# Performance work log

Measured on AMD Instinct MI355X. Metric: run time of the kernel, lower is better.

The kernel has to match this reference:

```python
import jax, jax.numpy as jnp
import numpy as np
from jax import lax

EPS = 1e-5
B, CIN, H, W = 4, 512, 64, 64
CI = CIN // 4          # inter_channels = 128
CQK = CI // 8          # PAM query/key channels = 16
NC = 19                # num_classes


def conv2d(x, w, pad):
    return lax.conv_general_dilated(x, w, (1, 1), [(pad, pad), (pad, pad)],
                                    dimension_numbers=('NCHW', 'OIHW', 'NCHW'))


def bn_relu(x, g, b, m, v):
    # eval-mode BatchNorm2d followed by ReLU
    inv = g * lax.rsqrt(v + EPS)
    return jax.nn.relu(x * inv[None, :, None, None] + (b - m * inv)[None, :, None, None])


def setup_inputs() -> dict:
    key = jax.random.key(0)
    ks = iter(jax.random.split(key, 40))
    rn = lambda shape, s=0.02: (jax.random.normal(next(ks), shape, dtype=jnp.float32) * s)
    ones = lambda n: jnp.ones((n,), jnp.float32)
    zeros = lambda n: jnp.zeros((n,), jnp.float32)
    inp = {
        'x': jax.random.normal(next(ks), (B, CIN, H, W), dtype=jnp.float32),
        # conv_p1: 3x3 conv (no bias) + BN
        'wp1': rn((CI, CIN, 3, 3)),
        'bnp1_w': ones(CI), 'bnp1_b': zeros(CI), 'bnp1_m': zeros(CI), 'bnp1_v': ones(CI),
        # PAM 1x1 convs
        'qw': rn((CQK, CI, 1, 1)), 'qb': zeros(CQK),
        'kw': rn((CQK, CI, 1, 1)), 'kb': zeros(CQK),
        'vw': rn((CI, CI, 1, 1)), 'vb': zeros(CI),
        'pam_gamma': jnp.full((1,), 0.5, jnp.float32),
        # conv_p2
        'wp2': rn((CI, CI, 3, 3)),
        'bnp2_w': ones(CI), 'bnp2_b': zeros(CI), 'bnp2_m': zeros(CI), 'bnp2_v': ones(CI),
        # conv_c1
        'wc1': rn((CI, CIN, 3, 3)),
        'bnc1_w': ones(CI), 'bnc1_b': zeros(CI), 'bnc1_m': zeros(CI), 'bnc1_v': ones(CI),
        'cam_gamma': jnp.full((1,), 0.5, jnp.float32),
        # conv_c2
        'wc2': rn((CI, CI, 3, 3)),
        'bnc2_w': ones(CI), 'bnc2_b': zeros(CI), 'bnc2_m': zeros(CI), 'bnc2_v': ones(CI),
        # classifier heads (dropout is eval-mode identity)
        'cls_w': rn((NC, CI, 1, 1)), 'cls_b': zeros(NC),
        'auxp_w': rn((NC, CI, 1, 1)), 'auxp_b': zeros(NC),
        'auxc_w': rn((NC, CI, 1, 1)), 'auxc_b': zeros(NC),
    }
    return inp


def pam(x, qw, qb, kw, kb, vw, vb, gamma):
    b, c, h, w = x.shape
    n = h * w
    q = (conv2d(x, qw, 0) + qb[None, :, None, None]).reshape(b, -1, n)  # [B,CQK,N]
    k = (conv2d(x, kw, 0) + kb[None, :, None, None]).reshape(b, -1, n)  # [B,CQK,N]
    v = (conv2d(x, vw, 0) + vb[None, :, None, None]).reshape(b, c, n)   # [B,C,N]
    attn = jax.nn.softmax(jnp.einsum('bcn,bcm->bnm', q, k), axis=-1)    # [B,N,N]
    out = jnp.einsum('bcm,bnm->bcn', v, attn).reshape(b, c, h, w)
    return gamma * out + x


def cam(x, gamma):
    b, c, h, w = x.shape
    f = x.reshape(b, c, -1)                                             # [B,C,N]
    attn = jax.nn.softmax(jnp.einsum('bin,bjn->bij', f, f), axis=-1)    # [B,C,C]
    out = jnp.einsum('bij,bjn->bin', attn, f).reshape(b, c, h, w)
    return gamma * out + x


def _forward(x, wp1, bnp1_w, bnp1_b, bnp1_m, bnp1_v,
             qw, qb, kw, kb, vw, vb, pam_gamma,
             wp2, bnp2_w, bnp2_b, bnp2_m, bnp2_v,
             wc1, bnc1_w, bnc1_b, bnc1_m, bnc1_v, cam_gamma,
             wc2, bnc2_w, bnc2_b, bnc2_m, bnc2_v,
             cls_w, cls_b, auxp_w, auxp_b, auxc_w, auxc_b):
    feat_p = bn_relu(conv2d(x, wp1, 1), bnp1_w, bnp1_b, bnp1_m, bnp1_v)
    feat_p = pam(feat_p, qw, qb, kw, kb, vw, vb, pam_gamma)
    feat_p = bn_relu(conv2d(feat_p, wp2, 1), bnp2_w, bnp2_b, bnp2_m, bnp2_v)

    feat_c = bn_relu(conv2d(x, wc1, 1), bnc1_w, bnc1_b, bnc1_m, bnc1_v)
    feat_c = cam(feat_c, cam_gamma)
    feat_c = bn_relu(conv2d(feat_c, wc2, 1), bnc2_w, bnc2_b, bnc2_m, bnc2_v)

    feat = feat_p + feat_c
    out = conv2d(feat, cls_w, 0) + cls_b[None, :, None, None]
    out_p = conv2d(feat_p, auxp_w, 0) + auxp_b[None, :, None, None]
    out_c = conv2d(feat_c, auxc_w, 0) + auxc_b[None, :, None, None]
    return out, out_p, out_c


def reference(x, wp1, bnp1_w, bnp1_b, bnp1_m, bnp1_v,
              qw, qb, kw, kb, vw, vb, pam_gamma,
              wp2, bnp2_w, bnp2_b, bnp2_m, bnp2_v,
              wc1, bnc1_w, bnc1_b, bnc1_m, bnc1_v, cam_gamma,
              wc2, bnc2_w, bnc2_b, bnc2_m, bnc2_v,
              cls_w, cls_b, auxp_w, auxp_b, auxc_w, auxc_b):
    return _forward(x, wp1, bnp1_w, bnp1_b, bnp1_m, bnp1_v,
                    qw, qb, kw, kb, vw, vb, pam_gamma,
                    wp2, bnp2_w, bnp2_b, bnp2_m, bnp2_v,
                    wc1, bnc1_w, bnc1_b, bnc1_m, bnc1_v, cam_gamma,
                    wc2, bnc2_w, bnc2_b, bnc2_m, bnc2_v,
                    cls_w, cls_b, auxp_w, auxp_b, auxc_w, auxc_b)
```

## Files before the change

### kernel.cpp

```cpp
#include <hip/hip_runtime.h>
#include <cstdint>
#include <cstddef>


using s16x8 = __attribute__((ext_vector_type(8))) short;
using u16x8 = __attribute__((ext_vector_type(8))) unsigned short;
using u16x4 = __attribute__((ext_vector_type(4))) unsigned short;
using f32x4 = __attribute__((ext_vector_type(4))) float;
using f32x16 = __attribute__((ext_vector_type(16))) float;
using u32x4v = __attribute__((ext_vector_type(4))) unsigned;

__device__ __forceinline__ f32x4 mfma16(u16x8 a, u16x8 b, f32x4 c) {
  return __builtin_amdgcn_mfma_f32_16x16x32_bf16(
      __builtin_bit_cast(s16x8, a), __builtin_bit_cast(s16x8, b), c, 0, 0, 0);
}
__device__ __forceinline__ f32x16 mfma32(u16x8 a, u16x8 b, f32x16 c) {
  return __builtin_amdgcn_mfma_f32_32x32x16_bf16(
      __builtin_bit_cast(s16x8, a), __builtin_bit_cast(s16x8, b), c, 0, 0, 0);
}
__device__ __forceinline__ float bf2f(unsigned short u) {
  return __builtin_bit_cast(float, (unsigned)u << 16);
}
__device__ __forceinline__ unsigned short f2bf(float f) {
  unsigned u = __builtin_bit_cast(unsigned, f);
  u += 0x7fffu + ((u >> 16) & 1u);
  return (unsigned short)(u >> 16);
}
__device__ __forceinline__ unsigned cvt_pk_bf16(float lo, float hi) {
  unsigned r;
  asm("v_cvt_pk_bf16_f32 %0, %1, %2" : "=v"(r) : "v"(lo), "v"(hi));
  return r;
}
__device__ __forceinline__ u16x8 ld8(const unsigned short* p) {
  return *reinterpret_cast<const u16x8*>(p);
}
__device__ __forceinline__ void gload16(const void* g, void* l) {
  __builtin_amdgcn_global_load_lds(
      (const __attribute__((address_space(1))) void*)g,
      (__attribute__((address_space(3))) void*)l, 16, 0, 0);
}

#define OFF_XT    ((size_t)0)
#define OFF_FP1   ((size_t)19464192)
#define OFF_FC1   ((size_t)24330240)
#define OFF_FP0   ((size_t)29196288)
#define OFF_FC0   ((size_t)33390592)
#define OFF_FP2   ((size_t)37584896)
#define OFF_FC2   ((size_t)41779200)
#define OFF_WT1   ((size_t)45973504)
#define OFF_WT2   ((size_t)48332800)
#define OFF_QKW   ((size_t)48922624)
#define OFF_VWW   ((size_t)48930816)
#define OFF_HWW   ((size_t)48963584)
#define OFF_BNSS  ((size_t)48988160)
#define OFF_ATTN  ((size_t)48992256)
#define OFF_Q     OFF_FP2
#define OFF_K     (OFF_FP2 + 524288)
#define OFF_V     OFF_FC2

__device__ __forceinline__ int swzkey8(int col) {
  return ((col ^ (col >> 3)) & 7) << 3;
}

__global__ __launch_bounds__(256) void k_padzero(char* ws0) {
  const int img = blockIdx.x;
  unsigned short* base;
  if (img < 32)
    base = (unsigned short*)(ws0 + OFF_XT) + (size_t)img * 304128;
  else if (img < 40)
    base = (unsigned short*)(ws0 + OFF_FP1) + (size_t)(img - 32) * 304128;
  else
    base = (unsigned short*)(ws0 + OFF_FC1) + (size_t)(img - 40) * 304128;
  const u16x8 z = {0, 0, 0, 0, 0, 0, 0, 0};
#pragma unroll 1
  for (int it = 0; it < 21; ++it) {
    int idx = it * 256 + threadIdx.x;
    if (idx >= 5248) break;
    int cell = idx >> 3, part = idx & 7;
    int row, col;
    if (cell < 72) {
      row = 0; col = cell;
    } else if (cell < 144) {
      row = 65; col = cell - 72;
    } else {
      int q = cell - 144;
      row = 1 + (q >> 3);
      int cc = q & 7;
      col = cc ? (64 + cc) : 0;
    }
    *(u16x8*)(base + (size_t)(row * 72 + col) * 64 + part * 8) = z;
  }
}

__global__ __launch_bounds__(256) void k_xpose(const float* __restrict__ x,
                                               unsigned short* __restrict__ xt) {
  __shared__ float tile[128][65];
  const int t = threadIdx.x;
  const int blk = blockIdx.x;
  const int cb = blk & 3;
  const int h = (blk >> 2) & 63;
  const int b = blk >> 8;
  const float* src = x + ((size_t)(b * 512 + cb * 128) * 64 + h) * 64;
  const int w = t & 63, cr = t >> 6;
  for (int i = 0; i < 32; ++i) tile[cr + i * 4][w] = src[(size_t)(cr + i * 4) * 4096 + w];
  __syncthreads();
  const int w2 = t >> 2, cg = t & 3;
  const int cic = cb * 2 + (cg >> 1);
  const int col = w2 + 1;
  const int key8 = swzkey8(col);
  unsigned short* dst =
      xt + (((size_t)(b * 8 + cic) * 66 + h + 1) * 72 + col) * 64 + (cg & 1) * 32;
#pragma unroll
  for (int j = 0; j < 32; j += 4) {
    const int q0 = (cg & 1) * 32 + j;
    const int srow = (cg >> 1) * 64 + (q0 ^ key8);
    u16x4 pk;
    pk[0] = f2bf(tile[srow + 0][w2]);
    pk[1] = f2bf(tile[srow + 1][w2]);
    pk[2] = f2bf(tile[srow + 2][w2]);
    pk[3] = f2bf(tile[srow + 3][w2]);
    *reinterpret_cast<u16x4*>(dst + j) = pk;
  }
}

struct PackArgs {
  const float *wp1, *wc1, *wp2, *wc2, *qw, *kw, *vw, *clsw, *apw, *acw;
  const float *g1p, *b1p, *m1p, *v1p, *g1c, *b1c, *m1c, *v1c;
  const float *g2p, *b2p, *m2p, *v2p, *g2c, *b2c, *m2c, *v2c;
  unsigned short *wt1, *wt2, *qkw, *vww, *hww;
  float* bnss;
};
__global__ __launch_bounds__(256) void k_pack(PackArgs A) {
  const int i = blockIdx.x * 256 + threadIdx.x;
  const int N1 = 2 * 8 * 9 * 8192;
  const int N2 = N1 + 2 * 2 * 9 * 8192;
  const int N3 = N2 + 2 * 16 * 128;
  const int N4 = N3 + 128 * 128;
  const int N5 = N4 + 3 * 32 * 128;
  const int N6 = N5 + 8 * 128;
  if (i < N1) {
    int e = i & 7, ln = (i >> 3) & 63, q = (i >> 9) & 15;
    int rest = i >> 13;
    int tap = rest % 9, cc = rest / 9;
    int cic = cc & 7, brr = cc >> 3;
    const float* s = brr ? A.wc1 : A.wp1;
    int co = (q >> 2) * 32 + (ln & 31);
    int ci = (q & 3) * 16 + (ln >> 5) * 8 + e;
    A.wt1[i] = f2bf(s[(size_t)(co * 512 + cic * 64 + ci) * 9 + tap]);
  } else if (i < N2) {
    int k = i - N1;
    int e = k & 7, ln = (k >> 3) & 63, q = (k >> 9) & 15;
    int rest = k >> 13;
    int tap = rest % 9, cc = rest / 9;
    int cic = cc & 1, brr = cc >> 1;
    const float* s = brr ? A.wc2 : A.wp2;
    int co = (q >> 2) * 32 + (ln & 31);
    int ci = (q & 3) * 16 + (ln >> 5) * 8 + e;
    A.wt2[k] = f2bf(s[(size_t)(co * 128 + cic * 64 + ci) * 9 + tap]);
  } else if (i < N3) {
    int k = i - N2;
    int ci = k & 127, q = k >> 7;
    const float* s = (q < 16) ? A.qw : A.kw;
    A.qkw[k] = f2bf(s[(q & 15) * 128 + ci]);
  } else if (i < N4) {
    int k = i - N3;
    A.vww[k] = f2bf(A.vw[k]);
  } else if (i < N5) {
    int k = i - N4;
    int ci = k & 127, co = (k >> 7) & 31, hd = k >> 12;
    const float* s = hd == 0 ? A.clsw : (hd == 1 ? A.apw : A.acw);
    A.hww[k] = (co < 19) ? f2bf(s[co * 128 + ci]) : (unsigned short)0;
  } else if (i < N6) {
    int k = i - N5;
    int j = k & 127, seg = k >> 7;
    const float *g, *bb, *mm, *vv;
    switch (seg >> 1) {
      case 0: g = A.g1p; bb = A.b1p; mm = A.m1p; vv = A.v1p; break;
      case 1: g = A.g1c; bb = A.b1c; mm = A.m1c; vv = A.v1c; break;
      case 2: g = A.g2p; bb = A.b2p; mm = A.m2p; vv = A.v2p; break;
      default: g = A.g2c; bb = A.b2c; mm = A.m2c; vv = A.v2c; break;
    }
    float sc = g[j] * rsqrtf(vv[j] + 1e-5f);
    A.bnss[k] = (seg & 1) ? (bb[j] - mm[j] * sc) : sc;
  }
}

__device__ __forceinline__ void conv_stageA(const unsigned short* inp, int imgChunk,
                                            int h0, int gtid, char* db) {
  const char* sr = (const char*)(inp + (((size_t)imgChunk * 66 + h0) * 72) * 64);
#pragma unroll
  for (int i = 0; i < 9; ++i)
    gload16(sr + i * 4096 + gtid * 16, db + i * 4096 + gtid * 16);
}

__device__ __forceinline__ void conv_loadW(const unsigned short* wgrp, int Tl, int wq,
                                           int lane, u16x8 (&s)[8]) {
  const unsigned short* wtap = wgrp + (size_t)Tl * 8192;
#pragma unroll
  for (int j = 0; j < 8; ++j)
    s[j] = ld8(wtap + (size_t)(wq + j) * 512 + lane * 8);
}

__device__ __forceinline__ void conv_tap(const char* ab, const unsigned short* wr,
                                         int wq, int lane, int l31, int hi16, int rowb,
                                         int ty, int tx, bool rld, u16x8 (&bvc)[8],
                                         f32x16& a00, f32x16& a01, f32x16& a10,
                                         f32x16& a11) {
  int abase0, akey0, abase1, akey1;
  {
    int col = l31 + tx;
    abase0 = ((rowb + ty) * 72 + col) << 7;
    akey0 = ((col ^ (col >> 3)) & 7) << 4;
    int col1 = 32 + l31 + tx;
    abase1 = ((rowb + ty) * 72 + col1) << 7;
    akey1 = ((col1 ^ (col1 >> 3)) & 7) << 4;
  }
#pragma unroll
  for (int s = 0; s < 4; ++s) {
    const int ko = s * 32 + hi16;
    u16x8 av0 = *(const u16x8*)(ab + abase0 + (ko ^ akey0));
    u16x8 av1 = *(const u16x8*)(ab + abase1 + (ko ^ akey1));
    a00 = mfma32(av0, bvc[s], a00);
    a01 = mfma32(av0, bvc[4 + s], a01);
    a10 = mfma32(av1, bvc[s], a10);
    a11 = mfma32(av1, bvc[4 + s], a11);
    if (rld) {
      bvc[s] = ld8(wr + (size_t)(wq + s) * 512 + lane * 8);
      bvc[4 + s] = ld8(wr + (size_t)(wq + 4 + s) * 512 + lane * 8);
    }
  }
}

__device__ __forceinline__ void acc_to_lds(f32x4* cbuf, int base, int lane,
                                           const f32x16& v) {
#pragma unroll
  for (int jj = 0; jj < 4; ++jj) {
    f32x4 x = {v[4 * jj + 0], v[4 * jj + 1], v[4 * jj + 2], v[4 * jj + 3]};
    cbuf[(base + jj) * 64 + lane] = x;
  }
}
__device__ __forceinline__ void acc_from_lds(const f32x4* cbuf, int base, int lane,
                                             f32x16& v) {
#pragma unroll
  for (int jj = 0; jj < 4; ++jj) {
    f32x4 x = cbuf[(base + jj) * 64 + lane];
#pragma unroll
    for (int r = 0; r < 4; ++r) v[4 * jj + r] += x[r];
  }
}
__device__ __forceinline__ void conv_store(unsigned short* outp, size_t bbase, int h0,
                                           int nbase, int co, float sc, float sh,
                                           int hi, const f32x16& v) {
#pragma unroll
  for (int r = 0; r < 16; ++r) {
    int n = nbase + (r & 3) + 8 * (r >> 2) + 4 * hi;
    float y = v[r] * sc + sh;
    y = y > 0.f ? y : 0.f;
    outp[bbase + ((size_t)(h0 + (n >> 6)) * 64 + (n & 63)) * 128 + co] = f2bf(y);
  }
}

template <int NCHUNK>
__global__ __launch_bounds__(512, 1) void k_conv3x3(
    const unsigned short* __restrict__ in0, const unsigned short* __restrict__ in1,
    const unsigned short* __restrict__ wt, const float* __restrict__ bnb,
    unsigned short* __restrict__ out0, unsigned short* __restrict__ out1) {
  __shared__ unsigned short Awin[2 * 4 * 72 * 64];
  const int bid = blockIdx.x;
  const int ht = bid & 31;
  const int b = (bid >> 5) & 3;
  const int br = bid >> 7;
  const unsigned short* inp = br ? in1 : in0;
  const unsigned short* wbr = wt + (size_t)br * NCHUNK * 9 * 8192;
  const float* scale = bnb + br * 256;
  const float* shiftp = scale + 128;
  unsigned short* outp = br ? out1 : out0;
  const int tid = threadIdx.x;
  const int lane = tid & 63, wv = tid >> 6;
  const int l31 = lane & 31, hi = lane >> 5;
  const int hi16 = hi * 16;
  const int group = wv >> 2, w = wv & 3;
  const int wn = (w & 1) * 64, cob = (w >> 1) * 64;
  const int rowb = w & 1;
  const int h0 = ht * 2;
  const int CPG = NCHUNK / 2;
  const int TPG = CPG * 9;
  const int c0 = group * CPG;
  const unsigned short* wgrp = wbr + (size_t)c0 * 9 * 8192;
  const int gtid = tid & 255;
  const int wq = (w >> 1) * 8;
  char* myA = (char*)Awin + group * 36864;
  const int imgBase = b * NCHUNK + c0;

  f32x16 a00 = (f32x16)0.f, a01 = (f32x16)0.f, a10 = (f32x16)0.f, a11 = (f32x16)0.f;
  u16x8 bv0[8], bv1[8];

  conv_stageA(inp, imgBase, h0, gtid, myA);
  conv_loadW(wgrp, 0, wq, lane, bv0);
  if (TPG > 1) conv_loadW(wgrp, 1, wq, lane, bv1);
  asm volatile("s_waitcnt vmcnt(0)" ::: "memory");
  __builtin_amdgcn_s_barrier();

#pragma unroll 1
  for (int c = 0; c < CPG; c += 2) {
#pragma unroll
    for (int t = 0; t < 9; ++t) {
      const int Tl = c * 9 + t;
      const bool rld = (Tl + 2 < TPG);
      const unsigned short* wr = wgrp + (size_t)(Tl + 2) * 8192;
      const int ty = t / 3, tx = t - ty * 3;
      if ((t & 1) == 0)
        conv_tap(myA, wr, wq, lane, l31, hi16, rowb, ty, tx, rld, bv0, a00, a01, a10, a11);
      else
        conv_tap(myA, wr, wq, lane, l31, hi16, rowb, ty, tx, rld, bv1, a00, a01, a10, a11);
    }
    if (c + 1 < CPG) {
      asm volatile("s_waitcnt lgkmcnt(0)" ::: "memory");
      __builtin_amdgcn_s_barrier();
      conv_stageA(inp, imgBase + c + 1, h0, gtid, myA);
      asm volatile("s_waitcnt vmcnt(0)" ::: "memory");
      __builtin_amdgcn_s_barrier();
#pragma unroll
      for (int t = 0; t < 9; ++t) {
        const int Tl = (c + 1) * 9 + t;
        const bool rld = (Tl + 2 < TPG);
        const unsigned short* wr = wgrp + (size_t)(Tl + 2) * 8192;
        const int ty = t / 3, tx = t - ty * 3;
        if ((t & 1) == 0)
          conv_tap(myA, wr, wq, lane, l31, hi16, rowb, ty, tx, rld, bv1, a00, a01, a10,
                   a11);
        else
          conv_tap(myA, wr, wq, lane, l31, hi16, rowb, ty, tx, rld, bv0, a00, a01, a10,
                   a11);
      }
      if (c + 2 < CPG) {
        asm volatile("s_waitcnt lgkmcnt(0)" ::: "memory");
        __builtin_amdgcn_s_barrier();
        conv_stageA(inp, imgBase + c + 2, h0, gtid, myA);
        asm volatile("s_waitcnt vmcnt(0)" ::: "memory");
        __builtin_amdgcn_s_barrier();
      }
    }
  }

  asm volatile("s_waitcnt lgkmcnt(0)" ::: "memory");
  __builtin_amdgcn_s_barrier();
  f32x4* cbuf = (f32x4*)Awin;
  if (group == 1) {
    acc_to_lds(cbuf, w * 16 + 0, lane, a00);
    acc_to_lds(cbuf, w * 16 + 4, lane, a01);
    acc_to_lds(cbuf, w * 16 + 8, lane, a10);
    acc_to_lds(cbuf, w * 16 + 12, lane, a11);
  }
  asm volatile("s_waitcnt lgkmcnt(0)" ::: "memory");
  __builtin_amdgcn_s_barrier();
  if (group == 0) {
    acc_from_lds(cbuf, w * 16 + 0, lane, a00);
    acc_from_lds(cbuf, w * 16 + 4, lane, a01);
    acc_from_lds(cbuf, w * 16 + 8, lane, a10);
    acc_from_lds(cbuf, w * 16 + 12, lane, a11);
    const size_t bbase = (size_t)b * 4096 * 128;
    {
      const int co = cob + l31;
      const float sc = scale[co], sh = shiftp[co];
      conv_store(outp, bbase, h0, wn + 0, co, sc, sh, hi, a00);
      conv_store(outp, bbase, h0, wn + 32, co, sc, sh, hi, a10);
    }
    {
      const int co = cob + 32 + l31;
      const float sc = scale[co], sh = shiftp[co];
      conv_store(outp, bbase, h0, wn + 0, co, sc, sh, hi, a01);
      conv_store(outp, bbase, h0, wn + 32, co, sc, sh, hi, a11);
    }
  }
}

__global__ __launch_bounds__(256) void k_qkv(
    const unsigned short* __restrict__ fp0, const unsigned short* __restrict__ qkw,
    const unsigned short* __restrict__ vww, const float* __restrict__ qb,
    const float* __restrict__ kb, const float* __restrict__ vb,
    unsigned short* __restrict__ Q, unsigned short* __restrict__ K,
    unsigned short* __restrict__ V2) {
  const int bid = blockIdx.x;
  const int nt = bid & 63, b = bid >> 6;
  const int lane = threadIdx.x & 63, wv = threadIdx.x >> 6;
  const int lg = lane >> 4, l15 = lane & 15;
  const int n = nt * 64 + wv * 16 + l15;
  const unsigned short* fbase = fp0 + ((size_t)b * 4096 + n) * 128 + lg * 8;
  f32x4 vacc[8];
#pragma unroll
  for (int mf = 0; mf < 8; ++mf) vacc[mf] = (f32x4){0.f, 0.f, 0.f, 0.f};
  f32x4 qacc = {0.f, 0.f, 0.f, 0.f}, kacc = {0.f, 0.f, 0.f, 0.f};
#pragma unroll
  for (int kc = 0; kc < 128; kc += 32) {
    u16x8 fb = ld8(fbase + kc);
    u16x8 qa = ld8(qkw + (size_t)l15 * 128 + lg * 8 + kc);
    u16x8 ka = ld8(qkw + 2048 + (size_t)l15 * 128 + lg * 8 + kc);
    qacc = mfma16(qa, fb, qacc);
    kacc = mfma16(ka, fb, kacc);
#pragma unroll
    for (int mf = 0; mf < 8; ++mf) {
      u16x8 va = ld8(vww + (size_t)(mf * 16 + l15) * 128 + lg * 8 + kc);
      vacc[mf] = mfma16(va, fb, vacc[mf]);
    }
  }
  const float LOG2E = 1.44269504088896f;
#pragma unroll
  for (int r = 0; r < 4; ++r) {
    int cq = lg * 4 + r;
    Q[(size_t)(b * 4096 + n) * 16 + cq] = f2bf((qacc[r] + qb[cq]) * LOG2E);
    K[(size_t)(b * 4096 + n) * 16 + cq] = f2bf(kacc[r] + kb[cq]);
  }
#pragma unroll
  for (int mf = 0; mf < 8; ++mf)
#pragma unroll
    for (int r = 0; r < 4; ++r) {
      int c = mf * 16 + lg * 4 + r;
      V2[((size_t)(b * 512 + (n >> 3)) * 128 + c) * 8 + (n & 7)] =
          f2bf(vacc[mf][r] + vb[c]);
    }
}

__global__ __launch_bounds__(512, 1) void k_pam(
    const unsigned short* __restrict__ Q, const unsigned short* __restrict__ K,
    const unsigned short* __restrict__ V2, const unsigned short* __restrict__ fp0,
    unsigned short* __restrict__ fp1, const float* __restrict__ pg) {
  __shared__ float obuf[2][3][16][64][4];
  __shared__ float lred[8][64];
  const int bid = blockIdx.x;
  const int qt = bid & 63, b = bid >> 6;
  const int tid = threadIdx.x;
  const int lane = tid & 63, wv = tid >> 6;
  const int qsub = wv >> 2, mq = wv & 3;
  const int l31 = lane & 31, hi = lane >> 5;
  const int q0 = qt * 64 + qsub * 32;
  const unsigned short* Qp = Q + (size_t)b * 65536;
  const unsigned short* Kp = K + (size_t)b * 65536;
  const unsigned short* Vp = V2 + (size_t)b * 524288;
  const int hi8 = hi * 8;

  const u16x8 qB = ld8(Qp + (size_t)(q0 + l31) * 16 + hi8);

  f32x16 oacc[4];
#pragma unroll
  for (int ch = 0; ch < 4; ++ch) oacc[ch] = (f32x16)0.f;
  float dsum = 0.f;

  auto loadK = [&](int t) -> u16x8 {
    return ld8(Kp + (size_t)(t * 32 + l31) * 16 + hi8);
  };
  auto loadV = [&](int t, u16x8 (&vf)[8]) {
#pragma unroll
    for (int kc = 0; kc < 2; ++kc)
#pragma unroll
      for (int ch = 0; ch < 4; ++ch)
        vf[kc * 4 + ch] =
            ld8(Vp + (size_t)(t * 4 + kc * 2 + hi) * 1024 + (ch * 32 + l31) * 8);
  };
  auto body = [&](u16x8 kA, u16x8 (&vf)[8]) {
    f32x16 pacc = mfma32(kA, qB, (f32x16)0.f);
    float p[16];
#pragma unroll
    for (int r = 0; r < 16; ++r) p[r] = exp2f(pacc[r]);
    dsum += (((p[0] + p[1]) + (p[2] + p[3])) + ((p[4] + p[5]) + (p[6] + p[7]))) +
            (((p[8] + p[9]) + (p[10] + p[11])) + ((p[12] + p[13]) + (p[14] + p[15])));
    unsigned X[8], S[8];
#pragma unroll
    for (int j = 0; j < 8; ++j) X[j] = cvt_pk_bf16(p[2 * j], p[2 * j + 1]);
#pragma unroll
    for (int j = 0; j < 8; ++j) S[j] = __shfl_xor(X[j], 32, 64);
    const bool hc = hi != 0;
    u32x4v w0, w1;
    w0[0] = hc ? S[2] : X[0];
    w0[1] = hc ? S[3] : X[1];
    w0[2] = hc ? X[2] : S[0];
    w0[3] = hc ? X[3] : S[1];
    w1[0] = hc ? S[6] : X[4];
    w1[1] = hc ? S[7] : X[5];
    w1[2] = hc ? X[6] : S[4];
    w1[3] = hc ? X[7] : S[5];
    u16x8 f0 = __builtin_bit_cast(u16x8, w0);
    u16x8 f1 = __builtin_bit_cast(u16x8, w1);
#pragma unroll
    for (int ch = 0; ch < 4; ++ch) oacc[ch] = mfma32(f0, vf[ch], oacc[ch]);
#pragma unroll
    for (int ch = 0; ch < 4; ++ch) oacc[ch] = mfma32(f1, vf[4 + ch], oacc[ch]);
  };

  const int t0 = mq * 32;
  u16x8 kA0 = loadK(t0), kA1;
  u16x8 vf0[8], vf1[8];
  loadV(t0, vf0);
#pragma unroll 1
  for (int t = 0; t < 32; t += 2) {
    kA1 = loadK(t0 + t + 1);
    loadV(t0 + t + 1, vf1);
    body(kA0, vf0);
    if (t + 2 < 32) {
      kA0 = loadK(t0 + t + 2);
      loadV(t0 + t + 2, vf0);
    }
    body(kA1, vf1);
  }

  dsum += __shfl_xor(dsum, 32, 64);
  lred[wv][lane] = dsum;
  if (mq) {
#pragma unroll
    for (int ch = 0; ch < 4; ++ch)
#pragma unroll
      for (int j = 0; j < 4; ++j) {
        f32x4 v = {oacc[ch][4 * j + 0], oacc[ch][4 * j + 1], oacc[ch][4 * j + 2],
                   oacc[ch][4 * j + 3]};
        *reinterpret_cast<f32x4*>(&obuf[qsub][mq - 1][ch * 4 + j][lane][0]) = v;
      }
  }
  __syncthreads();
  if (mq == 0) {
    const float dtot = lred[qsub * 4 + 0][lane] + lred[qsub * 4 + 1][lane] +
                       lred[qsub * 4 + 2][lane] + lred[qsub * 4 + 3][lane];
#pragma unroll
    for (int ch = 0; ch < 4; ++ch)
#pragma unroll
      for (int j = 0; j < 4; ++j) {
        f32x4 s0 = *reinterpret_cast<const f32x4*>(&obuf[qsub][0][ch * 4 + j][lane][0]);
        f32x4 s1 = *reinterpret_cast<const f32x4*>(&obuf[qsub][1][ch * 4 + j][lane][0]);
        f32x4 s2 = *reinterpret_cast<const f32x4*>(&obuf[qsub][2][ch * 4 + j][lane][0]);
#pragma unroll
        for (int r = 0; r < 4; ++r)
          oacc[ch][4 * j + r] += (s0[r] + s1[r]) + s2[r];
      }
    const float rden = 1.f / dtot;
    const float gm = pg[0];
    float rdr[16];
#pragma unroll
    for (int r = 0; r < 16; ++r)
      rdr[r] = __shfl(rden, (r & 3) + 8 * (r >> 2) + 4 * hi, 64);
#pragma unroll
    for (int ch = 0; ch < 4; ++ch) {
      const int c = ch * 32 + l31;
#pragma unroll
      for (int r = 0; r < 16; ++r) {
        const int n = q0 + (r & 3) + 8 * (r >> 2) + 4 * hi;
        const int wp = (n & 63) + 1;
        float o = gm * oacc[ch][r] * rdr[r] +
                  bf2f(fp0[((size_t)b * 4096 + n) * 128 + c]);
        fp1[(((size_t)(b * 2 + (c >> 6)) * 66 + (n >> 6) + 1) * 72 + wp) * 64 +
            ((c & 63) ^ swzkey8(wp))] = f2bf(o);
      }
    }
  }
}

__global__ __launch_bounds__(256) void k_gram(const unsigned short* __restrict__ fc0,
                                              float* __restrict__ Gp) {
  __shared__ float fl[32][132];
  const int bid = blockIdx.x;
  const int nc = bid & 63, b = bid >> 6;
  const int t = threadIdx.x;
  const int i = t >> 1, jh = (t & 1) * 64;
  float acc[64];
#pragma unroll
  for (int j = 0; j < 64; ++j) acc[j] = 0.f;
  for (int c2 = 0; c2 < 2; ++c2) {
    const int n0 = nc * 64 + c2 * 32;
    {
      int nn = t >> 3, kh = t & 7;
      const unsigned short* src = fc0 + ((size_t)b * 4096 + n0 + nn) * 128 + kh * 16;
      u16x8 v0 = ld8(src), v1 = ld8(src + 8);
#pragma unroll
      for (int e = 0; e < 8; ++e) {
        fl[nn][kh * 16 + e] = bf2f(v0[e]);
        fl[nn][kh * 16 + 8 + e] = bf2f(v1[e]);
      }
    }
    __syncthreads();
    for (int nn = 0; nn < 32; ++nn) {
      float fi = fl[nn][i];
      const float4* row = reinterpret_cast<const float4*>(&fl[nn][jh]);
#pragma unroll
      for (int j4 = 0; j4 < 16; ++j4) {
        float4 fv = row[j4];
        acc[4 * j4 + 0] += fi * fv.x;
        acc[4 * j4 + 1] += fi * fv.y;
        acc[4 * j4 + 2] += fi * fv.z;
        acc[4 * j4 + 3] += fi * fv.w;
      }
    }
    __syncthreads();
  }
  float* dst = Gp + (((size_t)b * 64 + nc) * 128 + i) * 128 + jh;
  float4* dst4 = reinterpret_cast<float4*>(dst);
#pragma unroll
  for (int j4 = 0; j4 < 16; ++j4)
    dst4[j4] = make_float4(acc[4 * j4], acc[4 * j4 + 1], acc[4 * j4 + 2], acc[4 * j4 + 3]);
}

__global__ __launch_bounds__(128) void k_softm(const float* __restrict__ Gp,
                                               unsigned short* __restrict__ attn) {
  const int bid = blockIdx.x;
  const int i = bid & 127, b = bid >> 7;
  const int j = threadIdx.x;
  float g = 0.f;
  for (int nc = 0; nc < 64; ++nc) g += Gp[(((size_t)b * 64 + nc) * 128 + i) * 128 + j];
  __shared__ float red[2], red2[2];
  float m = g;
  m = fmaxf(m, __shfl_xor(m, 1, 64));
  m = fmaxf(m, __shfl_xor(m, 2, 64));
  m = fmaxf(m, __shfl_xor(m, 4, 64));
  m = fmaxf(m, __shfl_xor(m, 8, 64));
  m = fmaxf(m, __shfl_xor(m, 16, 64));
  m = fmaxf(m, __shfl_xor(m, 32, 64));
  const int wvi = j >> 6;
  if ((j & 63) == 0) red[wvi] = m;
  __syncthreads();
  m = fmaxf(red[0], red[1]);
  float e = __expf(g - m);
  float s = e;
  s += __shfl_xor(s, 1, 64);
  s += __shfl_xor(s, 2, 64);
  s += __shfl_xor(s, 4, 64);
  s += __shfl_xor(s, 8, 64);
  s += __shfl_xor(s, 16, 64);
  s += __shfl_xor(s, 32, 64);
  if ((j & 63) == 0) red2[wvi] = s;
  __syncthreads();
  s = red2[0] + red2[1];
  attn[((size_t)b * 128 + i) * 128 + j] = f2bf(e / s);
}

__global__ __launch_bounds__(256) void k_camout(
    const unsigned short* __restrict__ fc0, const unsigned short* __restrict__ attn,
    const float* __restrict__ cg, unsigned short* __restrict__ fc1) {
  const int bid = blockIdx.x;
  const int nt = bid & 63, b = bid >> 6;
  const int lane = threadIdx.x & 63, wv = threadIdx.x >> 6;
  const int lg = lane >> 4, l15 = lane & 15;
  const int n = nt * 64 + wv * 16 + l15;
  const unsigned short* fbase = fc0 + ((size_t)b * 4096 + n) * 128 + lg * 8;
  const unsigned short* abase = attn + (size_t)b * 16384 + lg * 8;
  f32x4 acc[8];
#pragma unroll
  for (int mf = 0; mf < 8; ++mf) acc[mf] = (f32x4){0.f, 0.f, 0.f, 0.f};
#pragma unroll
  for (int kc = 0; kc < 128; kc += 32) {
    u16x8 fb = ld8(fbase + kc);
#pragma unroll
    for (int mf = 0; mf < 8; ++mf) {
      u16x8 aa = ld8(abase + (size_t)(mf * 16 + l15) * 128 + kc);
      acc[mf] = mfma16(aa, fb, acc[mf]);
    }
  }
  const float gm = cg[0];
  const int nn = nt * 64 + wv * 16 + l15;
  const int wp = (nn & 63) + 1;
  const int key8 = swzkey8(wp);
#pragma unroll
  for (int mf = 0; mf < 8; ++mf)
#pragma unroll
    for (int r = 0; r < 4; ++r) {
      int c = mf * 16 + lg * 4 + r;
      float o = gm * acc[mf][r] + bf2f(fc0[((size_t)b * 4096 + nn) * 128 + c]);
      fc1[(((size_t)(b * 2 + (c >> 6)) * 66 + (nn >> 6) + 1) * 72 + wp) * 64 +
          ((c & 63) ^ key8)] = f2bf(o);
    }
}

__global__ __launch_bounds__(256) void k_heads(
    const unsigned short* __restrict__ fp2, const unsigned short* __restrict__ fc2,
    const unsigned short* __restrict__ hw, const float* __restrict__ clsb,
    const float* __restrict__ apb, const float* __restrict__ acb,
    float* __restrict__ out) {
  const int bid = blockIdx.x;
  const int nt = bid & 63, b = bid >> 6;
  const int lane = threadIdx.x & 63, wv = threadIdx.x >> 6;
  const int lg = lane >> 4, l15 = lane & 15;
  const int n = nt * 64 + wv * 16 + l15;
  const unsigned short* pb = fp2 + (size_t)(b * 4096 + n) * 128 + lg * 8;
  const unsigned short* cb = fc2 + (size_t)(b * 4096 + n) * 128 + lg * 8;
  f32x4 acc[3][2];
#pragma unroll
  for (int hd = 0; hd < 3; ++hd)
#pragma unroll
    for (int mf = 0; mf < 2; ++mf) acc[hd][mf] = (f32x4){0.f, 0.f, 0.f, 0.f};
#pragma unroll
  for (int kc = 0; kc < 128; kc += 32) {
    u16x8 vp = ld8(pb + kc);
    u16x8 vc = ld8(cb + kc);
    u16x8 vs;
#pragma unroll
    for (int e = 0; e < 8; ++e) vs[e] = f2bf(bf2f(vp[e]) + bf2f(vc[e]));
#pragma unroll
    for (int mf = 0; mf < 2; ++mf) {
      u16x8 a0 = ld8(hw + (size_t)(0 * 32 + mf * 16 + l15) * 128 + lg * 8 + kc);
      u16x8 a1 = ld8(hw + (size_t)(1 * 32 + mf * 16 + l15) * 128 + lg * 8 + kc);
      u16x8 a2 = ld8(hw + (size_t)(2 * 32 + mf * 16 + l15) * 128 + lg * 8 + kc);
      acc[0][mf] = mfma16(a0, vs, acc[0][mf]);
      acc[1][mf] = mfma16(a1, vp, acc[1][mf]);
      acc[2][mf] = mfma16(a2, vc, acc[2][mf]);
    }
  }
  const float* bias[3] = {clsb, apb, acb};
  const size_t hoff[3] = {0, 311296, 622592};
#pragma unroll
  for (int hd = 0; hd < 3; ++hd)
#pragma unroll
    for (int mf = 0; mf < 2; ++mf)
#pragma unroll
      for (int r = 0; r < 4; ++r) {
        int co = mf * 16 + lg * 4 + r;
        if (co < 19)
          out[hoff[hd] + ((size_t)b * 19 + co) * 4096 + n] = acc[hd][mf][r] + bias[hd][co];
      }
}

extern "C" void kernel_launch(void* const* d_in, const int* in_sizes, int n_in,
                              void* d_out, int out_size, void* d_ws, size_t ws_size,
                              hipStream_t stream) {
  (void)in_sizes; (void)n_in; (void)out_size; (void)ws_size;
  const float* x = (const float*)d_in[0];
  const float* wp1 = (const float*)d_in[1];
  const float* g1p = (const float*)d_in[2];
  const float* b1p = (const float*)d_in[3];
  const float* m1p = (const float*)d_in[4];
  const float* v1p = (const float*)d_in[5];
  const float* qw = (const float*)d_in[6];
  const float* qb = (const float*)d_in[7];
  const float* kw = (const float*)d_in[8];
  const float* kb = (const float*)d_in[9];
  const float* vw = (const float*)d_in[10];
  const float* vb = (const float*)d_in[11];
  const float* pamg = (const float*)d_in[12];
  const float* wp2 = (const float*)d_in[13];
  const float* g2p = (const float*)d_in[14];
  const float* b2p = (const float*)d_in[15];
  const float* m2p = (const float*)d_in[16];
  const float* v2p = (const float*)d_in[17];
  const float* wc1 = (const float*)d_in[18];
  const float* g1c = (const float*)d_in[19];
  const float* b1c = (const float*)d_in[20];
  const float* m1c = (const float*)d_in[21];
  const float* v1c = (const float*)d_in[22];
  const float* camg = (const float*)d_in[23];
  const float* wc2 = (const float*)d_in[24];
  const float* g2c = (const float*)d_in[25];
  const float* b2c = (const float*)d_in[26];
  const float* m2c = (const float*)d_in[27];
  const float* v2c = (const float*)d_in[28];
  const float* clsw = (const float*)d_in[29];
  const float* clsb = (const float*)d_in[30];
  const float* apw = (const float*)d_in[31];
  const float* apb = (const float*)d_in[32];
  const float* acw = (const float*)d_in[33];
  const float* acb = (const float*)d_in[34];

  char* ws = (char*)d_ws;
  unsigned short* xt = (unsigned short*)(ws + OFF_XT);
  unsigned short* fp1 = (unsigned short*)(ws + OFF_FP1);
  unsigned short* fc1 = (unsigned short*)(ws + OFF_FC1);
  unsigned short* fp0 = (unsigned short*)(ws + OFF_FP0);
  unsigned short* fc0 = (unsigned short*)(ws + OFF_FC0);
  unsigned short* fp2 = (unsigned short*)(ws + OFF_FP2);
  unsigned short* fc2 = (unsigned short*)(ws + OFF_FC2);
  unsigned short* wt1 = (unsigned short*)(ws + OFF_WT1);
  unsigned short* wt2 = (unsigned short*)(ws + OFF_WT2);
  unsigned short* qkw = (unsigned short*)(ws + OFF_QKW);
  unsigned short* vww = (unsigned short*)(ws + OFF_VWW);
  unsigned short* hww = (unsigned short*)(ws + OFF_HWW);
  float* bnss = (float*)(ws + OFF_BNSS);
  unsigned short* Qb = (unsigned short*)(ws + OFF_Q);
  unsigned short* Kb = (unsigned short*)(ws + OFF_K);
  unsigned short* Vb = (unsigned short*)(ws + OFF_V);
  unsigned short* attnb = (unsigned short*)(ws + OFF_ATTN);
  float* Gp = (float*)(ws + OFF_XT);

  k_padzero<<<48, 256, 0, stream>>>(ws);

  PackArgs pa;
  pa.wp1 = wp1; pa.wc1 = wc1; pa.wp2 = wp2; pa.wc2 = wc2;
  pa.qw = qw; pa.kw = kw; pa.vw = vw; pa.clsw = clsw; pa.apw = apw; pa.acw = acw;
  pa.g1p = g1p; pa.b1p = b1p; pa.m1p = m1p; pa.v1p = v1p;
  pa.g1c = g1c; pa.b1c = b1c; pa.m1c = m1c; pa.v1c = v1c;
  pa.g2p = g2p; pa.b2p = b2p; pa.m2p = m2p; pa.v2p = v2p;
  pa.g2c = g2c; pa.b2c = b2c; pa.m2c = m2c; pa.v2c = v2c;
  pa.wt1 = wt1; pa.wt2 = wt2; pa.qkw = qkw; pa.vww = vww; pa.hww = hww; pa.bnss = bnss;
  k_pack<<<5892, 256, 0, stream>>>(pa);

  k_xpose<<<1024, 256, 0, stream>>>(x, xt);

  k_conv3x3<8><<<256, 512, 0, stream>>>(xt, xt, wt1, bnss, fp0, fc0);

  k_qkv<<<256, 256, 0, stream>>>(fp0, qkw, vww, qb, kb, vb, Qb, Kb, Vb);
  k_gram<<<256, 256, 0, stream>>>(fc0, Gp);
  k_pam<<<256, 512, 0, stream>>>(Qb, Kb, Vb, fp0, fp1, pamg);
  k_softm<<<512, 128, 0, stream>>>(Gp, attnb);
  k_camout<<<256, 256, 0, stream>>>(fc0, attnb, camg, fc1);

  k_conv3x3<2><<<256, 512, 0, stream>>>(fp1, fc1, wt2, bnss + 512, fp2, fc2);

  k_heads<<<256, 256, 0, stream>>>(fp2, fc2, hww, clsb, apb, acb, (float*)d_out);
}
```

Measured before the change: 207.1 us.

## Drop split-K wave groups in conv3x3, use 256-thread blocks

The 3x3 conv kernel previously split each block's input-channel chunks between two 4-wave groups and then reduced their partial accumulators through LDS. Now a single 4-wave group (256 threads) walks all channel chunks serially, so the LDS reduction, its extra barriers and half the LDS window are gone. The cost is half as many waves per block to hide latency, and a serial K loop twice as long per wave, with only 256 blocks on the device.

Result: slower. 211.9 us (+2.3%).

```diff
diff --git a/kernel.cpp b/kernel.cpp
--- a/kernel.cpp
+++ b/kernel.cpp
@@ -186,11 +186,11 @@
 }
 
 __device__ __forceinline__ void conv_stageA(const unsigned short* inp, int imgChunk,
-                                            int h0, int gtid, char* db) {
+                                            int h0, int tid, char* db) {
   const char* sr = (const char*)(inp + (((size_t)imgChunk * 66 + h0) * 72) * 64);
 #pragma unroll
   for (int i = 0; i < 9; ++i)
-    gload16(sr + i * 4096 + gtid * 16, db + i * 4096 + gtid * 16);
+    gload16(sr + i * 4096 + tid * 16, db + i * 4096 + tid * 16);
 }
 
 __device__ __forceinline__ void conv_loadW(const unsigned short* wgrp, int Tl, int wq,
@@ -231,23 +231,6 @@
   }
 }
 
-__device__ __forceinline__ void acc_to_lds(f32x4* cbuf, int base, int lane,
-                                           const f32x16& v) {
-#pragma unroll
-  for (int jj = 0; jj < 4; ++jj) {
-    f32x4 x = {v[4 * jj + 0], v[4 * jj + 1], v[4 * jj + 2], v[4 * jj + 3]};
-    cbuf[(base + jj) * 64 + lane] = x;
-  }
-}
-__device__ __forceinline__ void acc_from_lds(const f32x4* cbuf, int base, int lane,
-                                             f32x16& v) {
-#pragma unroll
-  for (int jj = 0; jj < 4; ++jj) {
-    f32x4 x = cbuf[(base + jj) * 64 + lane];
-#pragma unroll
-    for (int r = 0; r < 4; ++r) v[4 * jj + r] += x[r];
-  }
-}
 __device__ __forceinline__ void conv_store(unsigned short* outp, size_t bbase, int h0,
                                            int nbase, int co, float sc, float sh,
                                            int hi, const f32x16& v) {
@@ -261,11 +244,11 @@
 }
 
 template <int NCHUNK>
-__global__ __launch_bounds__(512, 1) void k_conv3x3(
+__global__ __launch_bounds__(256, 1) void k_conv3x3(
     const unsigned short* __restrict__ in0, const unsigned short* __restrict__ in1,
     const unsigned short* __restrict__ wt, const float* __restrict__ bnb,
     unsigned short* __restrict__ out0, unsigned short* __restrict__ out1) {
-  __shared__ unsigned short Awin[2 * 4 * 72 * 64];
+  __shared__ unsigned short Awin[4 * 72 * 64];
   const int bid = blockIdx.x;
   const int ht = bid & 31;
   const int b = (bid >> 5) & 3;
@@ -279,52 +262,47 @@
   const int lane = tid & 63, wv = tid >> 6;
   const int l31 = lane & 31, hi = lane >> 5;
   const int hi16 = hi * 16;
-  const int group = wv >> 2, w = wv & 3;
-  const int wn = (w & 1) * 64, cob = (w >> 1) * 64;
-  const int rowb = w & 1;
+  const int wn = (wv & 1) * 64, cob = (wv >> 1) * 64;
+  const int rowb = wv & 1;
   const int h0 = ht * 2;
-  const int CPG = NCHUNK / 2;
-  const int TPG = CPG * 9;
-  const int c0 = group * CPG;
-  const unsigned short* wgrp = wbr + (size_t)c0 * 9 * 8192;
-  const int gtid = tid & 255;
-  const int wq = (w >> 1) * 8;
-  char* myA = (char*)Awin + group * 36864;
-  const int imgBase = b * NCHUNK + c0;
+  const int TT = NCHUNK * 9;
+  const int wq = (wv >> 1) * 8;
+  char* myA = (char*)Awin;
+  const int imgBase = b * NCHUNK;
 
   f32x16 a00 = (f32x16)0.f, a01 = (f32x16)0.f, a10 = (f32x16)0.f, a11 = (f32x16)0.f;
   u16x8 bv0[8], bv1[8];
 
-  conv_stageA(inp, imgBase, h0, gtid, myA);
-  conv_loadW(wgrp, 0, wq, lane, bv0);
-  if (TPG > 1) conv_loadW(wgrp, 1, wq, lane, bv1);
+  conv_stageA(inp, imgBase, h0, tid, myA);
+  conv_loadW(wbr, 0, wq, lane, bv0);
+  conv_loadW(wbr, 1, wq, lane, bv1);
   asm volatile("s_waitcnt vmcnt(0)" ::: "memory");
   __builtin_amdgcn_s_barrier();
 
 #pragma unroll 1
-  for (int c = 0; c < CPG; c += 2) {
+  for (int c = 0; c < NCHUNK; c += 2) {
 #pragma unroll
     for (int t = 0; t < 9; ++t) {
       const int Tl = c * 9 + t;
-      const bool rld = (Tl + 2 < TPG);
-      const unsigned short* wr = wgrp + (size_t)(Tl + 2) * 8192;
+      const bool rld = (Tl + 2 < TT);
+      const unsigned short* wr = wbr + (size_t)(Tl + 2) * 8192;
       const int ty = t / 3, tx = t - ty * 3;
       if ((t & 1) == 0)
         conv_tap(myA, wr, wq, lane, l31, hi16, rowb, ty, tx, rld, bv0, a00, a01, a10, a11);
       else
         conv_tap(myA, wr, wq, lane, l31, hi16, rowb, ty, tx, rld, bv1, a00, a01, a10, a11);
     }
-    if (c + 1 < CPG) {
+    if (c + 1 < NCHUNK) {
       asm volatile("s_waitcnt lgkmcnt(0)" ::: "memory");
       __builtin_amdgcn_s_barrier();
-      conv_stageA(inp, imgBase + c + 1, h0, gtid, myA);
+      conv_stageA(inp, imgBase + c + 1, h0, tid, myA);
       asm volatile("s_waitcnt vmcnt(0)" ::: "memory");
       __builtin_amdgcn_s_barrier();
 #pragma unroll
       for (int t = 0; t < 9; ++t) {
         const int Tl = (c + 1) * 9 + t;
-        const bool rld = (Tl + 2 < TPG);
-        const unsigned short* wr = wgrp + (size_t)(Tl + 2) * 8192;
+        const bool rld = (Tl + 2 < TT);
+        const unsigned short* wr = wbr + (size_t)(Tl + 2) * 8192;
         const int ty = t / 3, tx = t - ty * 3;
         if ((t & 1) == 0)
           conv_tap(myA, wr, wq, lane, l31, hi16, rowb, ty, tx, rld, bv1, a00, a01, a10,
@@ -333,45 +311,28 @@
           conv_tap(myA, wr, wq, lane, l31, hi16, rowb, ty, tx, rld, bv0, a00, a01, a10,
                    a11);
       }
-      if (c + 2 < CPG) {
+      if (c + 2 < NCHUNK) {
         asm volatile("s_waitcnt lgkmcnt(0)" ::: "memory");
         __builtin_amdgcn_s_barrier();
-        conv_stageA(inp, imgBase + c + 2, h0, gtid, myA);
+        conv_stageA(inp, imgBase + c + 2, h0, tid, myA);
         asm volatile("s_waitcnt vmcnt(0)" ::: "memory");
         __builtin_amdgcn_s_barrier();
       }
     }
   }
 
-  asm volatile("s_waitcnt lgkmcnt(0)" ::: "memory");
-  __builtin_amdgcn_s_barrier();
-  f32x4* cbuf = (f32x4*)Awin;
-  if (group == 1) {
-    acc_to_lds(cbuf, w * 16 + 0, lane, a00);
-    acc_to_lds(cbuf, w * 16 + 4, lane, a01);
-    acc_to_lds(cbuf, w * 16 + 8, lane, a10);
-    acc_to_lds(cbuf, w * 16 + 12, lane, a11);
-  }
-  asm volatile("s_waitcnt lgkmcnt(0)" ::: "memory");
-  __builtin_amdgcn_s_barrier();
-  if (group == 0) {
-    acc_from_lds(cbuf, w * 16 + 0, lane, a00);
-    acc_from_lds(cbuf, w * 16 + 4, lane, a01);
-    acc_from_lds(cbuf, w * 16 + 8, lane, a10);
-    acc_from_lds(cbuf, w * 16 + 12, lane, a11);
-    const size_t bbase = (size_t)b * 4096 * 128;
-    {
-      const int co = cob + l31;
-      const float sc = scale[co], sh = shiftp[co];
-      conv_store(outp, bbase, h0, wn + 0, co, sc, sh, hi, a00);
-      conv_store(outp, bbase, h0, wn + 32, co, sc, sh, hi, a10);
-    }
-    {
-      const int co = cob + 32 + l31;
-      const float sc = scale[co], sh = shiftp[co];
-      conv_store(outp, bbase, h0, wn + 0, co, sc, sh, hi, a01);
-      conv_store(outp, bbase, h0, wn + 32, co, sc, sh, hi, a11);
-    }
+  const size_t bbase = (size_t)b * 4096 * 128;
+  {
+    const int co = cob + l31;
+    const float sc = scale[co], sh = shiftp[co];
+    conv_store(outp, bbase, h0, wn + 0, co, sc, sh, hi, a00);
+    conv_store(outp, bbase, h0, wn + 32, co, sc, sh, hi, a10);
+  }
+  {
+    const int co = cob + 32 + l31;
+    const float sc = scale[co], sh = shiftp[co];
+    conv_store(outp, bbase, h0, wn + 0, co, sc, sh, hi, a01);
+    conv_store(outp, bbase, h0, wn + 32, co, sc, sh, hi, a11);
   }
 }
 
@@ -788,7 +749,7 @@
 
   k_xpose<<<1024, 256, 0, stream>>>(x, xt);
 
-  k_conv3x3<8><<<256, 512, 0, stream>>>(xt, xt, wt1, bnss, fp0, fc0);
+  k_conv3x3<8><<<256, 256, 0, stream>>>(xt, xt, wt1, bnss, fp0, fc0);
 
   k_qkv<<<256, 256, 0, stream>>>(fp0, qkw, vww, qb, kb, vb, Qb, Kb, Vb);
   k_gram<<<256, 256, 0, stream>>>(fc0, Gp);
@@ -796,7 +757,7 @@
   k_softm<<<512, 128, 0, stream>>>(Gp, attnb);
   k_camout<<<256, 256, 0, stream>>>(fc0, attnb, camg, fc1);
 
-  k_conv3x3<2><<<256, 512, 0, stream>>>(fp1, fc1, wt2, bnss + 512, fp2, fc2);
+  k_conv3x3<2><<<256, 256, 0, stream>>>(fp1, fc1, wt2, bnss + 512, fp2, fc2);
 
   k_heads<<<256, 256, 0, stream>>>(fp2, fc2, hww, clsb, apb, acb, (float*)d_out);
 }
```
